# Performance work log

Measured on AMD Instinct MI355X. Metric: run time of the kernel, lower is better.

The kernel has to match this reference:

```python
import jax, jax.numpy as jnp
import numpy as np

EPS = 1e-5
DN = ('NCDHW', 'OIDHW', 'NCDHW')

def conv3d(x, w, b):
    y = jax.lax.conv_general_dilated(x, w, (1, 1, 1), 'SAME', dimension_numbers=DN)
    return y + b[None, :, None, None, None]

def batchnorm(x, gamma, beta):
    # training-mode BatchNorm3d: biased batch stats over (N, D, H, W) per channel
    mean = jnp.mean(x, axis=(0, 2, 3, 4), keepdims=True)
    var = jnp.mean((x - mean) ** 2, axis=(0, 2, 3, 4), keepdims=True)
    xhat = (x - mean) * jax.lax.rsqrt(var + EPS)
    return gamma[None, :, None, None, None] * xhat + beta[None, :, None, None, None]

def setup_inputs() -> dict:
    key = jax.random.key(0)
    ks = jax.random.split(key, 8)
    C, N = 32, 4  # channel, fuzzynum
    B, D, H, W = 4, 64, 64, 64
    x = jax.random.normal(ks[0], (B, C, D, H, W), dtype=jnp.float32)
    fan1 = C * 27
    conv1_w = jax.random.uniform(ks[1], (1, C, 3, 3, 3), jnp.float32, -1, 1) / np.sqrt(fan1)
    conv1_b = jnp.zeros((1,), jnp.float32)
    fan2 = 1 * 27
    conv2_w = jax.random.uniform(ks[2], (C, 1, 3, 3, 3), jnp.float32, -1, 1) / np.sqrt(fan2)
    conv2_b = jnp.zeros((C,), jnp.float32)
    mu = jax.random.normal(ks[3], (C, N), dtype=jnp.float32)
    sigma = jax.random.normal(ks[4], (C, N), dtype=jnp.float32)
    bn1_g = jnp.ones((1,), jnp.float32)
    bn1_b = jnp.zeros((1,), jnp.float32)
    bn2_g = jnp.ones((C,), jnp.float32)
    bn2_b = jnp.zeros((C,), jnp.float32)
    return {"x": x, "conv1_w": conv1_w, "conv1_b": conv1_b, "conv2_w": conv2_w,
            "conv2_b": conv2_b, "mu": mu, "sigma": sigma,
            "bn1_g": bn1_g, "bn1_b": bn1_b, "bn2_g": bn2_g, "bn2_b": bn2_b}

def reference(x, conv1_w, conv1_b, conv2_w, conv2_b, mu, sigma, bn1_g, bn1_b, bn2_g, bn2_b):
    x1 = conv3d(x, conv1_w, conv1_b)                      # [B,1,D,H,W]
    # fuzzy Gaussian membership: only channel 0 of mu/sigma is used (x1 has 1 channel)
    m = mu[0]                                             # [n]
    s = sigma[0]                                          # [n]
    z = (x1[..., None] - m) / s                           # [B,1,D,H,W,n]
    fuzz = jnp.exp(-jnp.sum(z * z, axis=-1))              # [B,1,D,H,W]
    y = batchnorm(fuzz, bn1_g, bn1_b)
    y = conv3d(y, conv2_w, conv2_b)                       # [B,C,D,H,W]
    return batchnorm(y, bn2_g, bn2_b)
```

## Files before the change

### kernel.cpp

```cpp
#include <hip/hip_runtime.h>

constexpr int Cc = 32;
constexpr int SP = 64 * 64 * 64;
constexpr int TS = 4 * SP;

constexpr int PW  = 68;
constexpr int PZR = 66 * PW;
constexpr int PSP = 66 * PZR;
constexpr int PTOT = 4 * PSP;

constexpr int ACC_N = 68 + 64 * 64;

__global__ __launch_bounds__(256) void k_conv1_fuzzy(
    const float* __restrict__ x, const float* __restrict__ w1,
    const float* __restrict__ b1, const float* __restrict__ mu,
    const float* __restrict__ sg, float* __restrict__ fuzz,
    float* __restrict__ acc)
{
    const int tid = threadIdx.x;
    const int t = blockIdx.x * 256 + tid;
    const int wq = t & 15;        const int w0 = wq << 2;
    const int zp = (t >> 4) & 31; const int z0 = zp << 1;
    const int y  = (t >> 9) & 63;
    const int b  = t >> 15;
    const int lane = tid & 63;

    float S1 = 0.f, S2 = 0.f, S3 = 0.f;
#pragma unroll
    for (int n = 0; n < 4; n++) {
        float m = mu[n], s = sg[n];
        float iv = 1.0f / (s * s);
        S1 += iv; S2 += m * iv; S3 += m * m * iv;
    }

    const float b1v = b1[0];
    float a00 = b1v, a01 = b1v, a02 = b1v, a03 = b1v;
    float a10 = b1v, a11 = b1v, a12 = b1v, a13 = b1v;

    const float* xb = x + (size_t)b * Cc * SP;

    bool pv[12]; int ofs[12];
#pragma unroll
    for (int rz = 0; rz < 4; rz++) {
        const int zz = z0 - 1 + rz;
        const int zzc = min(max(zz, 0), 63);
        const bool okz = (unsigned)zz < 64u;
#pragma unroll
        for (int dy = 0; dy < 3; dy++) {
            const int yy = y - 1 + dy;
            const int yyc = min(max(yy, 0), 63);
            pv[rz * 3 + dy]  = okz && ((unsigned)yy < 64u);
            ofs[rz * 3 + dy] = (zzc << 12) + (yyc << 6) + w0;
        }
    }

    auto LOADCH = [&](int c, float4 (&M)[12]) {
        const float* xc = xb + (size_t)c * SP;
#pragma unroll
        for (int i = 0; i < 12; i++)
            M[i] = *(const float4*)(xc + ofs[i]);
    };

    auto COMPUTECH = [&](int c, float4 (&M)[12]) {
#pragma unroll
        for (int i = 0; i < 12; i++) {
            if (true) {
                M[i].x = pv[i] ? M[i].x : 0.f;
                M[i].y = pv[i] ? M[i].y : 0.f;
                M[i].z = pv[i] ? M[i].z : 0.f;
                M[i].w = pv[i] ? M[i].w : 0.f;
            }
        }
        const float* wc = w1 + c * 27;
        float Wv[27];
#pragma unroll
        for (int k = 0; k < 27; k++) Wv[k] = wc[k];
#pragma unroll
        for (int rz = 0; rz < 4; rz++) {
#pragma unroll
            for (int dy = 0; dy < 3; dy++) {
                const float4 m = M[rz * 3 + dy];
                const float lv = __shfl(m.w, (lane + 63) & 63, 64);
                const float rv = __shfl(m.x, (lane + 1) & 63, 64);
                const float v0 = (wq > 0)  ? lv : 0.f;
                const float v5 = (wq < 15) ? rv : 0.f;
                const float v1 = m.x, v2 = m.y, v3 = m.z, v4 = m.w;
                if (rz < 3) {
                    const float W0 = Wv[(rz*3+dy)*3], W1 = Wv[(rz*3+dy)*3+1], W2 = Wv[(rz*3+dy)*3+2];
                    a00 = fmaf(v0, W0, fmaf(v1, W1, fmaf(v2, W2, a00)));
                    a01 = fmaf(v1, W0, fmaf(v2, W1, fmaf(v3, W2, a01)));
                    a02 = fmaf(v2, W0, fmaf(v3, W1, fmaf(v4, W2, a02)));
                    a03 = fmaf(v3, W0, fmaf(v4, W1, fmaf(v5, W2, a03)));
                }
                if (rz >= 1) {
                    const float W0 = Wv[((rz-1)*3+dy)*3], W1 = Wv[((rz-1)*3+dy)*3+1], W2 = Wv[((rz-1)*3+dy)*3+2];
                    a10 = fmaf(v0, W0, fmaf(v1, W1, fmaf(v2, W2, a10)));
                    a11 = fmaf(v1, W0, fmaf(v2, W1, fmaf(v3, W2, a11)));
                    a12 = fmaf(v2, W0, fmaf(v3, W1, fmaf(v4, W2, a12)));
                    a13 = fmaf(v3, W0, fmaf(v4, W1, fmaf(v5, W2, a13)));
                }
            }
        }
    };

    float4 Ma[12], Mb[12];
    LOADCH(0, Ma);
    for (int c = 0; c < Cc; c += 2) {
        LOADCH(c + 1, Mb);
        COMPUTECH(c, Ma);
        if (c + 2 < Cc) LOADCH(c + 2, Ma);
        COMPUTECH(c + 1, Mb);
    }

    float fsum = 0.f, fsq = 0.f;
#pragma unroll
    for (int oz = 0; oz < 2; oz++) {
        float xv[4] = { oz ? a10 : a00, oz ? a11 : a01,
                        oz ? a12 : a02, oz ? a13 : a03 };
        float* fp = fuzz + (size_t)b * PSP + (size_t)(z0 + oz + 1) * PZR
                  + (y + 1) * PW + (w0 + 1);
#pragma unroll
        for (int ow = 0; ow < 4; ow++) {
            float x1 = xv[ow];
            float tt = x1 * x1 * S1 - 2.0f * x1 * S2 + S3;
            float fz = __expf(-tt);
            fp[ow] = fz; fsum += fz; fsq += fz * fz;
        }
    }
#pragma unroll
    for (int m = 1; m < 64; m <<= 1) {
        fsum += __shfl_xor(fsum, m, 64);
        fsq  += __shfl_xor(fsq,  m, 64);
    }
    __shared__ float red[8];
    const int wid = tid >> 6;
    if ((tid & 63) == 0) { red[wid * 2] = fsum; red[wid * 2 + 1] = fsq; }
    __syncthreads();
    if (tid == 0) {
        atomicAdd(&acc[0], red[0] + red[2] + red[4] + red[6]);
        atomicAdd(&acc[1], red[1] + red[3] + red[5] + red[7]);
    }
}

__global__ void k_fin1(const float* __restrict__ g, const float* __restrict__ be,
                       float* __restrict__ acc)
{
    float mean = acc[0] * (1.0f / TS);
    float var  = acc[1] * (1.0f / TS) - mean * mean;
    float a = g[0] * rsqrtf(var + 1e-5f);
    acc[2] = a;
    acc[3] = be[0] - mean * a;
}

__global__ __launch_bounds__(256) void k_bn1_apply(
    float* __restrict__ fuzz, const float* __restrict__ acc)
{
    const int t = blockIdx.x * 256 + threadIdx.x;
    if (t >= PTOT) return;
    const int b  = t / PSP;  const int r  = t - b * PSP;
    const int zp = r / PZR;  const int r2 = r - zp * PZR;
    const int yp = r2 / PW;  const int wp = r2 - yp * PW;
    const bool inter = ((unsigned)(zp - 1) < 64u) &&
                       ((unsigned)(yp - 1) < 64u) &&
                       ((unsigned)(wp - 1) < 64u);
    const float a = acc[2], sh = acc[3];
    const float v = fuzz[t];
    fuzz[t] = inter ? fmaf(a, v, sh) : 0.f;
}

__global__ __launch_bounds__(256) void k_conv2_fused(
    const float* __restrict__ fuzz, const float* __restrict__ w2,
    const float* __restrict__ b2, float* __restrict__ acc,
    float* __restrict__ out)
{
    const int tid = threadIdx.x;
    const int lane = tid & 63;
    const int wid = tid >> 6;
    const int bi = blockIdx.x;
    const int w = lane;
    const int y = bi & 63;
    const int z0 = ((bi >> 6) & 15) << 2;
    const int b = bi >> 10;
    const float* fb = fuzz + (size_t)b * PSP;

    float Fl[6][3], Fm[6][3], Fr[6][3];
#pragma unroll
    for (int rz = 0; rz < 6; rz++) {
#pragma unroll
        for (int dy = 0; dy < 3; dy++) {
            const float* rp = fb + (size_t)(z0 + rz) * PZR + (y + dy) * PW + w;
            Fl[rz][dy] = rp[0];
            Fm[rz][dy] = rp[1];
            Fr[rz][dy] = rp[2];
        }
    }

    float* ob = out + (size_t)b * Cc * SP + (z0 << 12) + (y << 6) + w;
    const int slot = bi & 63;
    const int c0 = wid * 8;

#pragma unroll
    for (int ci = 0; ci < 8; ci++) {
        const int c = c0 + ci;
        const float* wc = w2 + c * 27;
        float Wv[27];
#pragma unroll
        for (int k = 0; k < 27; k++) Wv[k] = wc[k];
        const float bb = b2[c];
        float o0 = bb, o1 = bb, o2 = bb, o3 = bb;
#pragma unroll
        for (int rz = 0; rz < 6; rz++) {
#pragma unroll
            for (int dy = 0; dy < 3; dy++) {
                const float l = Fl[rz][dy], m = Fm[rz][dy], r = Fr[rz][dy];
#pragma unroll
                for (int oz = 0; oz < 4; oz++) {
                    const int dz = rz - oz;
                    if (dz < 0 || dz > 2) continue;
                    const float W0 = Wv[(dz*3+dy)*3], W1 = Wv[(dz*3+dy)*3+1], W2 = Wv[(dz*3+dy)*3+2];
                    if      (oz == 0) o0 = fmaf(l, W0, fmaf(m, W1, fmaf(r, W2, o0)));
                    else if (oz == 1) o1 = fmaf(l, W0, fmaf(m, W1, fmaf(r, W2, o1)));
                    else if (oz == 2) o2 = fmaf(l, W0, fmaf(m, W1, fmaf(r, W2, o2)));
                    else              o3 = fmaf(l, W0, fmaf(m, W1, fmaf(r, W2, o3)));
                }
            }
        }
        ob[(size_t)c * SP]         = o0;
        ob[(size_t)c * SP + 4096]  = o1;
        ob[(size_t)c * SP + 8192]  = o2;
        ob[(size_t)c * SP + 12288] = o3;

        float ps = (o0 + o1) + (o2 + o3);
        float pq = fmaf(o0, o0, fmaf(o1, o1, fmaf(o2, o2, o3 * o3)));
#pragma unroll
        for (int mm = 1; mm < 64; mm <<= 1) {
            ps += __shfl_xor(ps, mm, 64);
            pq += __shfl_xor(pq, mm, 64);
        }
        if (lane == 0) {
            atomicAdd(&acc[68 + c * 64 + slot], ps);
            atomicAdd(&acc[68 + (32 + c) * 64 + slot], pq);
        }
    }
}

__global__ void k_fin2(const float* __restrict__ g, const float* __restrict__ be,
                       float* __restrict__ acc)
{
    int c = threadIdx.x;
    float s = 0.f, q = 0.f;
    for (int k = 0; k < 64; k++) {
        s += acc[68 + c * 64 + k];
        q += acc[68 + (32 + c) * 64 + k];
    }
    float mean = s * (1.0f / TS);
    float var  = q * (1.0f / TS) - mean * mean;
    float sc = g[c] * rsqrtf(var + 1e-5f);
    acc[4 + c]  = sc;
    acc[36 + c] = be[c] - mean * sc;
}

__global__ __launch_bounds__(256) void k_bn2_apply(
    const float* __restrict__ acc, float* __restrict__ out)
{
    const int t = blockIdx.x * 256 + threadIdx.x;
    const int c = (t >> 16) & 31;
    const float sc = acc[4 + c], sh = acc[36 + c];
    float4 v = ((const float4*)out)[t];
    v.x = fmaf(v.x, sc, sh);
    v.y = fmaf(v.y, sc, sh);
    v.z = fmaf(v.z, sc, sh);
    v.w = fmaf(v.w, sc, sh);
    ((float4*)out)[t] = v;
}

extern "C" void kernel_launch(void* const* d_in, const int* in_sizes, int n_in,
                              void* d_out, int out_size, void* d_ws, size_t ws_size,
                              hipStream_t stream)
{
    const float* x   = (const float*)d_in[0];
    const float* w1  = (const float*)d_in[1];
    const float* b1  = (const float*)d_in[2];
    const float* w2  = (const float*)d_in[3];
    const float* b2  = (const float*)d_in[4];
    const float* mu  = (const float*)d_in[5];
    const float* sg  = (const float*)d_in[6];
    const float* g1  = (const float*)d_in[7];
    const float* be1 = (const float*)d_in[8];
    const float* g2  = (const float*)d_in[9];
    const float* be2 = (const float*)d_in[10];

    float* out  = (float*)d_out;
    float* fuzz = (float*)d_ws;
    float* acc  = fuzz + PTOT;

    hipMemsetAsync(acc, 0, ACC_N * sizeof(float), stream);
    k_conv1_fuzzy<<<512, 256, 0, stream>>>(x, w1, b1, mu, sg, fuzz, acc);
    k_fin1<<<1, 1, 0, stream>>>(g1, be1, acc);
    k_bn1_apply<<<(PTOT + 255) / 256, 256, 0, stream>>>(fuzz, acc);
    k_conv2_fused<<<4096, 256, 0, stream>>>(fuzz, w2, b2, acc, out);
    k_fin2<<<1, 32, 0, stream>>>(g2, be2, acc);
    k_bn2_apply<<<32768, 256, 0, stream>>>(acc, out);
}
```

Before: 378.4 us.

## Fold BN1 affine into conv2 via border weight sums and recompute conv2 instead of rereading output

Removes the BN1 apply pass by running conv2 on raw fuzz values and correcting with the BN1 scale plus shift times per-position-class sums of conv2 weights, which are precomputed in fin1. Conv2 now runs twice: a first pass only accumulates BN2 statistics, and a second pass recomputes the convolution and writes the normalized output directly. This drops the 128MB write-then-read-modify-write pass over the output. The cost is a second full conv2 compute and a full memset of the padded fuzz buffer, which the padding now relies on to be zero. The conv1 channel loop is also deepened to a 4-buffer prefetch.

```diff
diff --git a/kernel.cpp b/kernel.cpp
--- a/kernel.cpp
+++ b/kernel.cpp
@@ -9,7 +9,8 @@
 constexpr int PSP = 66 * PZR;
 constexpr int PTOT = 4 * PSP;
 
-constexpr int ACC_N = 68 + 64 * 64;
+constexpr int WOFF  = 68 + 64 * 64;
+constexpr int ACC_N = WOFF + 864;
 
 __global__ __launch_bounds__(256) void k_conv1_fuzzy(
     const float* __restrict__ x, const float* __restrict__ w1,
@@ -64,12 +65,10 @@
     auto COMPUTECH = [&](int c, float4 (&M)[12]) {
 #pragma unroll
         for (int i = 0; i < 12; i++) {
-            if (true) {
-                M[i].x = pv[i] ? M[i].x : 0.f;
-                M[i].y = pv[i] ? M[i].y : 0.f;
-                M[i].z = pv[i] ? M[i].z : 0.f;
-                M[i].w = pv[i] ? M[i].w : 0.f;
-            }
+            M[i].x = pv[i] ? M[i].x : 0.f;
+            M[i].y = pv[i] ? M[i].y : 0.f;
+            M[i].z = pv[i] ? M[i].z : 0.f;
+            M[i].w = pv[i] ? M[i].w : 0.f;
         }
         const float* wc = w1 + c * 27;
         float Wv[27];
@@ -103,13 +102,18 @@
         }
     };
 
-    float4 Ma[12], Mb[12];
-    LOADCH(0, Ma);
-    for (int c = 0; c < Cc; c += 2) {
-        LOADCH(c + 1, Mb);
-        COMPUTECH(c, Ma);
-        if (c + 2 < Cc) LOADCH(c + 2, Ma);
-        COMPUTECH(c + 1, Mb);
+    float4 Ba[12], Bb[12], Bc[12], Bd[12];
+    LOADCH(0, Ba);
+    LOADCH(1, Bb);
+    for (int c = 0; c < Cc; c += 4) {
+        LOADCH(c + 2, Bc);
+        COMPUTECH(c, Ba);
+        LOADCH(c + 3, Bd);
+        COMPUTECH(c + 1, Bb);
+        if (c + 4 < Cc) LOADCH(c + 4, Ba);
+        COMPUTECH(c + 2, Bc);
+        if (c + 5 < Cc) LOADCH(c + 5, Bb);
+        COMPUTECH(c + 3, Bd);
     }
 
     float fsum = 0.f, fsq = 0.f;
@@ -143,32 +147,43 @@
 }
 
 __global__ void k_fin1(const float* __restrict__ g, const float* __restrict__ be,
-                       float* __restrict__ acc)
-{
-    float mean = acc[0] * (1.0f / TS);
-    float var  = acc[1] * (1.0f / TS) - mean * mean;
-    float a = g[0] * rsqrtf(var + 1e-5f);
-    acc[2] = a;
-    acc[3] = be[0] - mean * a;
-}
-
-__global__ __launch_bounds__(256) void k_bn1_apply(
-    float* __restrict__ fuzz, const float* __restrict__ acc)
-{
-    const int t = blockIdx.x * 256 + threadIdx.x;
-    if (t >= PTOT) return;
-    const int b  = t / PSP;  const int r  = t - b * PSP;
-    const int zp = r / PZR;  const int r2 = r - zp * PZR;
-    const int yp = r2 / PW;  const int wp = r2 - yp * PW;
-    const bool inter = ((unsigned)(zp - 1) < 64u) &&
-                       ((unsigned)(yp - 1) < 64u) &&
-                       ((unsigned)(wp - 1) < 64u);
-    const float a = acc[2], sh = acc[3];
-    const float v = fuzz[t];
-    fuzz[t] = inter ? fmaf(a, v, sh) : 0.f;
-}
-
-__global__ __launch_bounds__(256) void k_conv2_fused(
+                       const float* __restrict__ w2, float* __restrict__ acc)
+{
+    const int tid = threadIdx.x;
+    if (tid == 0) {
+        float mean = acc[0] * (1.0f / TS);
+        float var  = acc[1] * (1.0f / TS) - mean * mean;
+        float a = g[0] * rsqrtf(var + 1e-5f);
+        acc[2] = a;
+        acc[3] = be[0] - mean * a;
+    }
+    if (tid < 864) {
+        const int c   = tid / 27;
+        const int cls = tid - c * 27;
+        const int zc  = cls / 9;
+        const int r   = cls - zc * 9;
+        const int yc  = r / 3;
+        const int xc  = r - yc * 3;
+        float s = 0.f;
+#pragma unroll
+        for (int dz = 0; dz < 3; dz++) {
+            if ((zc == 0 && dz == 0) || (zc == 2 && dz == 2)) continue;
+#pragma unroll
+            for (int dy = 0; dy < 3; dy++) {
+                if ((yc == 0 && dy == 0) || (yc == 2 && dy == 2)) continue;
+#pragma unroll
+                for (int dx = 0; dx < 3; dx++) {
+                    if ((xc == 0 && dx == 0) || (xc == 2 && dx == 2)) continue;
+                    s += w2[c * 27 + (dz * 3 + dy) * 3 + dx];
+                }
+            }
+        }
+        acc[WOFF + tid] = s;
+    }
+}
+
+template <bool WRITE>
+__global__ __launch_bounds__(256) void k_conv2(
     const float* __restrict__ fuzz, const float* __restrict__ w2,
     const float* __restrict__ b2, float* __restrict__ acc,
     float* __restrict__ out)
@@ -181,6 +196,7 @@
     const int y = bi & 63;
     const int z0 = ((bi >> 6) & 15) << 2;
     const int b = bi >> 10;
+    const float a = acc[2], sh = acc[3];
     const float* fb = fuzz + (size_t)b * PSP;
 
     float Fl[6][3], Fm[6][3], Fr[6][3];
@@ -195,6 +211,11 @@
         }
     }
 
+    const int yc  = (y == 0) ? 0 : ((y == 63) ? 2 : 1);
+    const int zc0 = (z0 == 0) ? 0 : 1;
+    const int zc3 = (z0 + 3 == 63) ? 2 : 1;
+    const bool lo = (lane == 0), hi = (lane == 63);
+
     float* ob = out + (size_t)b * Cc * SP + (z0 << 12) + (y << 6) + w;
     const int slot = bi & 63;
     const int c0 = wid * 8;
@@ -206,8 +227,7 @@
         float Wv[27];
 #pragma unroll
         for (int k = 0; k < 27; k++) Wv[k] = wc[k];
-        const float bb = b2[c];
-        float o0 = bb, o1 = bb, o2 = bb, o3 = bb;
+        float o0 = 0.f, o1 = 0.f, o2 = 0.f, o3 = 0.f;
 #pragma unroll
         for (int rz = 0; rz < 6; rz++) {
 #pragma unroll
@@ -225,21 +245,40 @@
                 }
             }
         }
-        ob[(size_t)c * SP]         = o0;
-        ob[(size_t)c * SP + 4096]  = o1;
-        ob[(size_t)c * SP + 8192]  = o2;
-        ob[(size_t)c * SP + 12288] = o3;
-
-        float ps = (o0 + o1) + (o2 + o3);
-        float pq = fmaf(o0, o0, fmaf(o1, o1, fmaf(o2, o2, o3 * o3)));
-#pragma unroll
-        for (int mm = 1; mm < 64; mm <<= 1) {
-            ps += __shfl_xor(ps, mm, 64);
-            pq += __shfl_xor(pq, mm, 64);
-        }
-        if (lane == 0) {
-            atomicAdd(&acc[68 + c * 64 + slot], ps);
-            atomicAdd(&acc[68 + (32 + c) * 64 + slot], pq);
+        const float bb = b2[c];
+        const float* tb = acc + WOFF + c * 27 + yc * 3;
+        const float* t0 = tb + zc0 * 9;
+        const float* t1 = tb + 9;
+        const float* t3 = tb + zc3 * 9;
+        const float w0s = lo ? t0[0] : (hi ? t0[2] : t0[1]);
+        const float w1s = lo ? t1[0] : (hi ? t1[2] : t1[1]);
+        const float w3s = lo ? t3[0] : (hi ? t3[2] : t3[1]);
+        const float off0 = fmaf(sh, w0s, bb);
+        const float off1 = fmaf(sh, w1s, bb);
+        const float off3 = fmaf(sh, w3s, bb);
+        const float v0 = fmaf(o0, a, off0);
+        const float v1 = fmaf(o1, a, off1);
+        const float v2 = fmaf(o2, a, off1);
+        const float v3 = fmaf(o3, a, off3);
+
+        if (WRITE) {
+            const float sc = acc[4 + c], s2 = acc[36 + c];
+            ob[(size_t)c * SP]         = fmaf(v0, sc, s2);
+            ob[(size_t)c * SP + 4096]  = fmaf(v1, sc, s2);
+            ob[(size_t)c * SP + 8192]  = fmaf(v2, sc, s2);
+            ob[(size_t)c * SP + 12288] = fmaf(v3, sc, s2);
+        } else {
+            float ps = (v0 + v1) + (v2 + v3);
+            float pq = fmaf(v0, v0, fmaf(v1, v1, fmaf(v2, v2, v3 * v3)));
+#pragma unroll
+            for (int mm = 1; mm < 64; mm <<= 1) {
+                ps += __shfl_xor(ps, mm, 64);
+                pq += __shfl_xor(pq, mm, 64);
+            }
+            if (lane == 0) {
+                atomicAdd(&acc[68 + c * 64 + slot], ps);
+                atomicAdd(&acc[68 + (32 + c) * 64 + slot], pq);
+            }
         }
     }
 }
@@ -247,31 +286,22 @@
 __global__ void k_fin2(const float* __restrict__ g, const float* __restrict__ be,
                        float* __restrict__ acc)
 {
-    int c = threadIdx.x;
-    float s = 0.f, q = 0.f;
-    for (int k = 0; k < 64; k++) {
-        s += acc[68 + c * 64 + k];
-        q += acc[68 + (32 + c) * 64 + k];
-    }
-    float mean = s * (1.0f / TS);
-    float var  = q * (1.0f / TS) - mean * mean;
-    float sc = g[c] * rsqrtf(var + 1e-5f);
-    acc[4 + c]  = sc;
-    acc[36 + c] = be[c] - mean * sc;
-}
-
-__global__ __launch_bounds__(256) void k_bn2_apply(
-    const float* __restrict__ acc, float* __restrict__ out)
-{
-    const int t = blockIdx.x * 256 + threadIdx.x;
-    const int c = (t >> 16) & 31;
-    const float sc = acc[4 + c], sh = acc[36 + c];
-    float4 v = ((const float4*)out)[t];
-    v.x = fmaf(v.x, sc, sh);
-    v.y = fmaf(v.y, sc, sh);
-    v.z = fmaf(v.z, sc, sh);
-    v.w = fmaf(v.w, sc, sh);
-    ((float4*)out)[t] = v;
+    const int tid = threadIdx.x;
+    const int c = tid >> 5, j = tid & 31;
+    float s = acc[68 + c * 64 + j]        + acc[68 + c * 64 + 32 + j];
+    float q = acc[68 + (32 + c) * 64 + j] + acc[68 + (32 + c) * 64 + 32 + j];
+#pragma unroll
+    for (int m = 1; m < 32; m <<= 1) {
+        s += __shfl_xor(s, m, 32);
+        q += __shfl_xor(q, m, 32);
+    }
+    if (j == 0) {
+        float mean = s * (1.0f / TS);
+        float var  = q * (1.0f / TS) - mean * mean;
+        float sc = g[c] * rsqrtf(var + 1e-5f);
+        acc[4 + c]  = sc;
+        acc[36 + c] = be[c] - mean * sc;
+    }
 }
 
 extern "C" void kernel_launch(void* const* d_in, const int* in_sizes, int n_in,
@@ -294,11 +324,10 @@
     float* fuzz = (float*)d_ws;
     float* acc  = fuzz + PTOT;
 
-    hipMemsetAsync(acc, 0, ACC_N * sizeof(float), stream);
+    hipMemsetAsync(fuzz, 0, (size_t)(PTOT + ACC_N) * sizeof(float), stream);
     k_conv1_fuzzy<<<512, 256, 0, stream>>>(x, w1, b1, mu, sg, fuzz, acc);
-    k_fin1<<<1, 1, 0, stream>>>(g1, be1, acc);
-    k_bn1_apply<<<(PTOT + 255) / 256, 256, 0, stream>>>(fuzz, acc);
-    k_conv2_fused<<<4096, 256, 0, stream>>>(fuzz, w2, b2, acc, out);
-    k_fin2<<<1, 32, 0, stream>>>(g2, be2, acc);
-    k_bn2_apply<<<32768, 256, 0, stream>>>(acc, out);
-}
+    k_fin1<<<1, 864, 0, stream>>>(g1, be1, w2, acc);
+    k_conv2<false><<<4096, 256, 0, stream>>>(fuzz, w2, b2, acc, out);
+    k_fin2<<<1, 1024, 0, stream>>>(g2, be2, acc);
+    k_conv2<true><<<4096, 256, 0, stream>>>(fuzz, w2, b2, acc, out);
+}
```

Result: slower. 406.3 us (+7.4%).
